# Performance work log

Hardware: AMD Instinct MI355X
Metric: run time of the kernel (lower is better)

Reference implementation:

```python
import jax, jax.numpy as jnp
import numpy as np

CHANNELS = 512
NUM_HEADS = 8
GROUPS = 32
EPS = 1e-5


def setup_inputs() -> dict:
    key = jax.random.key(0)
    ks = jax.random.split(key, 7)
    C = CHANNELS
    x = jax.random.normal(ks[0], (8, C, 32, 32), dtype=jnp.float32)
    gn_weight = jnp.ones((C,), dtype=jnp.float32)
    gn_bias = jnp.zeros((C,), dtype=jnp.float32)
    # Conv1d(C, 3C, k=1) weights ~ N(0, 0.02) per init_weights
    qkv_w = 0.02 * jax.random.normal(ks[1], (3 * C, C), dtype=jnp.float32)
    qkv_b = 0.01 * jax.random.normal(ks[2], (3 * C,), dtype=jnp.float32)
    out_w = 0.02 * jax.random.normal(ks[3], (C, C), dtype=jnp.float32)
    out_b = 0.01 * jax.random.normal(ks[4], (C,), dtype=jnp.float32)
    return {"x": x, "gn_weight": gn_weight, "gn_bias": gn_bias,
            "qkv_w": qkv_w, "qkv_b": qkv_b, "out_w": out_w, "out_b": out_b}


def _forward(x, gn_weight, gn_bias, qkv_w, qkv_b, out_w, out_b):
    n, c, h, w = x.shape
    hw = h * w
    heads = NUM_HEADS
    cph = c // heads
    xs = x.reshape(n, c, hw)  # [N, C, HW]
    # GroupNorm over (channels-in-group, spatial)
    xg = xs.reshape(n, GROUPS, c // GROUPS, hw)
    mean = jnp.mean(xg, axis=(2, 3), keepdims=True)
    var = jnp.var(xg, axis=(2, 3), keepdims=True)
    xn = ((xg - mean) * jax.lax.rsqrt(var + EPS)).reshape(n, c, hw)
    xn = xn * gn_weight[None, :, None] + gn_bias[None, :, None]
    # 1x1 Conv1d QKV projection
    qkv = jnp.einsum('oc,ncl->nol', qkv_w, xn) + qkv_b[None, :, None]  # [N, 3C, HW]
    q, k, v = jnp.split(qkv, 3, axis=1)  # each [N, C, HW]
    q = q.reshape(n * heads, cph, hw)
    k = k.reshape(n * heads, cph, hw)
    v = v.reshape(n * heads, cph, hw)
    scale = 1.0 / np.sqrt(cph).astype(np.float32)
    scores = jnp.einsum('bci,bcj->bij', q, k) * scale  # [NH, HW, HW]
    attn = jax.nn.softmax(scores, axis=-1)
    weighted = jnp.einsum('bij,bcj->bic', attn, v)  # [NH, HW, cph]
    # Faithful to torch: reshape(n, -1, h, w) on [n*heads, hw, cph] layout
    weighted = weighted.reshape(n, c, h, w)
    out = jnp.einsum('oc,nchw->nohw', out_w, weighted) + out_b[None, :, None, None]
    return out


def reference(x, gn_weight, gn_bias, qkv_w, qkv_b, out_w, out_b):
    return _forward(x, gn_weight, gn_bias, qkv_w, qkv_b, out_w, out_b)
```

## Files before the change

### kernel.cpp

```cpp
#include <hip/hip_runtime.h>
#include <math.h>

#define N_    8
#define C_    512
#define HW_   1024
#define G_    32
#define CPG_  16
#define OC3_  1536
#define LOG2E 1.44269504f

typedef _Float16 f16;
typedef f16 f16x8 __attribute__((ext_vector_type(8)));
typedef f16 f16x4 __attribute__((ext_vector_type(4)));
typedef float f32x4 __attribute__((ext_vector_type(4)));

#define GLOAD_LDS16(g, l)                                                          \
    __builtin_amdgcn_global_load_lds(                                              \
        (const __attribute__((address_space(1))) unsigned int*)(const void*)(g),   \
        (__attribute__((address_space(3))) unsigned int*)(void*)(l), 16, 0, 0)

#define WAIT_VM0() __builtin_amdgcn_s_waitcnt(0x0F70)

__global__ __launch_bounds__(256) void prep(const float* __restrict__ x,
                                            const float* __restrict__ gw,
                                            const float* __restrict__ gb,
                                            f16* __restrict__ XT,
                                            const float* __restrict__ qkv_w,
                                            const float* __restrict__ out_w,
                                            const float* __restrict__ qkv_b,
                                            f16* __restrict__ Wq,
                                            f16* __restrict__ Wo,
                                            float* __restrict__ qkv_bs) {
    __shared__ float red1[4], red2[4];
    __shared__ float sm, srstd;
    if (blockIdx.x >= 256) {
        const float QS = 0.125f * LOG2E;
        int idx = (blockIdx.x - 256) * 256 + threadIdx.x;
        if (idx < 786432) {
            float v = qkv_w[idx];
            if (idx < 262144) v *= QS;
            Wq[idx] = (f16)v;
        } else if (idx < 786432 + 262144) {
            Wo[idx - 786432] = (f16)out_w[idx - 786432];
        } else if (idx < 786432 + 262144 + 1536) {
            int i = idx - 786432 - 262144;
            float v = qkv_b[i];
            if (i < 512) v *= QS;
            qkv_bs[i] = v;
        }
        return;
    }
    int blk = blockIdx.x;
    int n = blk >> 5, g = blk & 31;
    size_t base = ((size_t)n * C_ + (size_t)g * CPG_) * HW_;
    const float4* xp4 = (const float4*)(x + base);
    float4 vals[16];
    float s1 = 0.f, s2 = 0.f;
#pragma unroll
    for (int r = 0; r < 16; r++) {
        float4 v = xp4[r * 256 + threadIdx.x];
        vals[r] = v;
        s1 += v.x + v.y + v.z + v.w;
        s2 += v.x * v.x + v.y * v.y + v.z * v.z + v.w * v.w;
    }
#pragma unroll
    for (int off = 32; off > 0; off >>= 1) {
        s1 += __shfl_down(s1, off, 64);
        s2 += __shfl_down(s2, off, 64);
    }
    int wave = threadIdx.x >> 6, lane = threadIdx.x & 63;
    if (lane == 0) { red1[wave] = s1; red2[wave] = s2; }
    __syncthreads();
    if (threadIdx.x == 0) {
        float t1 = red1[0] + red1[1] + red1[2] + red1[3];
        float t2 = red2[0] + red2[1] + red2[2] + red2[3];
        float mean = t1 * (1.f / 16384.f);
        float var  = t2 * (1.f / 16384.f) - mean * mean;
        sm = mean;
        srstd = rsqrtf(var + 1e-5f);
    }
    __syncthreads();
    float mean = sm, rstd = srstd;
    float av[16], bbv[16];
#pragma unroll
    for (int r = 0; r < 16; r++) {
        int c = g * CPG_ + r;
        av[r] = gw[c] * rstd;
        bbv[r] = gb[c] - mean * av[r];
    }
    f16x8 lo[4], hi[4];
#pragma unroll
    for (int r = 0; r < 16; r++) {
        float4 v = vals[r];
        float a = av[r], bb = bbv[r];
        f16 e0 = (f16)(v.x * a + bb), e1 = (f16)(v.y * a + bb);
        f16 e2 = (f16)(v.z * a + bb), e3 = (f16)(v.w * a + bb);
        if (r < 8) { lo[0][r] = e0; lo[1][r] = e1; lo[2][r] = e2; lo[3][r] = e3; }
        else { hi[0][r - 8] = e0; hi[1][r - 8] = e1; hi[2][r - 8] = e2; hi[3][r - 8] = e3; }
    }
    f16* xt = XT + (size_t)n * C_ * HW_ + ((size_t)g * HW_ + threadIdx.x * 4) * 16;
#pragma unroll
    for (int comp = 0; comp < 4; comp++) {
        *(f16x8*)&xt[comp * 16]     = lo[comp];
        *(f16x8*)&xt[comp * 16 + 8] = hi[comp];
    }
}

template <bool FINAL>
__global__ __launch_bounds__(256, 4) void gemm_f16(const f16* __restrict__ A,
                                                   const f16* __restrict__ B,
                                                   const float* __restrict__ bias,
                                                   void* __restrict__ Yq,
                                                   f16* __restrict__ Yv) {
    constexpr int BM = FINAL ? 64 : 128;
    constexpr int MI = BM / 32;
    constexpr int AB = BM * 64;
    __shared__ __align__(16) unsigned char smem[FINAL ? 24576 : 34816];
    int tid = threadIdx.x, lane = tid & 63, w = tid >> 6;
    int m = lane & 15, quad = lane >> 4;
    int ow0 = (w & 1) * (BM / 2), lw0 = (w >> 1) * 64;
    int flat = blockIdx.x;
    int n = flat & 7, rest = flat >> 3;
    int l0 = (rest & 7) * 128, o0 = (rest >> 3) * BM;
    const f16* Bn = B + (size_t)n * C_ * HW_;

    f32x4 acc[MI][4];
#pragma unroll
    for (int i = 0; i < MI; i++)
#pragma unroll
        for (int j = 0; j < 4; j++)
#pragma unroll
            for (int r = 0; r < 4; r++) acc[i][j][r] = 0.f;

#define STAGE_STEP(c0_, pb_)                                                       \
    do {                                                                           \
        _Pragma("unroll")                                                          \
        for (int it = 0; it < BM / 64; it++) {                                     \
            int q = it * 256 + tid;                                                \
            int row = q >> 2, sg = (q & 3) ^ ((row >> 1) & 3);                     \
            GLOAD_LDS16(A + (size_t)(o0 + row) * 512 + (c0_) + sg * 8,             \
                        (f16*)(smem + (pb_) * AB) + (size_t)(it * 256 + w * 64) * 8); \
        }                                                                          \
        _Pragma("unroll")                                                          \
        for (int it = 0; it < 2; it++) {                                           \
            int q = it * 256 + tid;                                                \
            int row = q >> 2, sg = (q & 3) ^ ((row >> 1) & 3);                     \
            size_t baddr;                                                          \
            if (FINAL) {                                                           \
                baddr = (size_t)(l0 + row) * 512 + (c0_) + sg * 8;                 \
            } else {                                                               \
                int c = (c0_) + sg * 8;                                            \
                baddr = ((size_t)(c >> 4) * HW_ + (l0 + row)) * 16 + (c & 15);     \
            }                                                                      \
            GLOAD_LDS16(Bn + baddr,                                                \
                        (f16*)(smem + 2 * AB + (pb_) * 8192) +                     \
                            (size_t)(it * 256 + w * 64) * 8);                      \
        }                                                                          \
    } while (0)

    STAGE_STEP(0, 0);

    for (int cs = 0; cs < 16; cs++) {
        int p = cs & 1;
        WAIT_VM0();
        __syncthreads();
        if (cs < 15) STAGE_STEP((cs + 1) * 32, 1 - p);
        const f16* Asp = (const f16*)(smem + p * AB);
        const f16* Bsp = (const f16*)(smem + 2 * AB + p * 8192);
        f16x8 af[MI], bf[4];
#pragma unroll
        for (int ib = 0; ib < MI; ib++) {
            int row = ow0 + ib * 16 + m;
            int sg = quad ^ ((row >> 1) & 3);
            af[ib] = *(const f16x8*)&Asp[row * 32 + sg * 8];
        }
#pragma unroll
        for (int jb = 0; jb < 4; jb++) {
            int row = lw0 + jb * 16 + m;
            int sg = quad ^ ((row >> 1) & 3);
            bf[jb] = *(const f16x8*)&Bsp[row * 32 + sg * 8];
        }
#pragma unroll
        for (int ib = 0; ib < MI; ib++)
#pragma unroll
            for (int jb = 0; jb < 4; jb++)
                acc[ib][jb] = __builtin_amdgcn_mfma_f32_16x16x32_f16(
                    af[ib], bf[jb], acc[ib][jb], 0, 0, 0);
    }
#undef STAGE_STEP

    float bv[MI][4];
#pragma unroll
    for (int ib = 0; ib < MI; ib++)
#pragma unroll
        for (int r = 0; r < 4; r++)
            bv[ib][r] = bias[o0 + ow0 + ib * 16 + quad * 4 + r];

    if (FINAL) {
        float* on = (float*)Yq + (size_t)n * C_ * HW_;
#pragma unroll
        for (int ib = 0; ib < MI; ib++)
#pragma unroll
            for (int jb = 0; jb < 4; jb++)
#pragma unroll
                for (int r = 0; r < 4; r++)
                    on[(size_t)(o0 + ow0 + ib * 16 + quad * 4 + r) * HW_ +
                       l0 + lw0 + jb * 16 + m] = acc[ib][jb][r] + bv[ib][r];
    } else if (o0 >= 1024) {
        f16* vn = Yv + (size_t)n * C_ * HW_;
#pragma unroll
        for (int ib = 0; ib < MI; ib++)
#pragma unroll
            for (int jb = 0; jb < 4; jb++)
#pragma unroll
                for (int r = 0; r < 4; r++)
                    vn[(size_t)(o0 - 1024 + ow0 + ib * 16 + quad * 4 + r) * HW_ +
                       l0 + lw0 + jb * 16 + m] = (f16)(acc[ib][jb][r] + bv[ib][r]);
    } else {
        __syncthreads();
        f16* T = (f16*)smem;
#pragma unroll
        for (int ib = 0; ib < MI; ib++)
#pragma unroll
            for (int jb = 0; jb < 4; jb++) {
                f16x4 h;
#pragma unroll
                for (int r = 0; r < 4; r++) h[r] = (f16)(acc[ib][jb][r] + bv[ib][r]);
                int l = lw0 + jb * 16 + m;
                int oo = ow0 + ib * 16 + quad * 4;
                *(f16x4*)&T[l * 136 + oo] = h;
            }
        __syncthreads();
        f16* qn = (f16*)Yq + (size_t)n * HW_ * 1024;
#pragma unroll
        for (int rep = 0; rep < 8; rep++) {
            int idx = rep * 256 + tid;
            int l = idx >> 4, seg = idx & 15;
            f16x8 v = *(const f16x8*)&T[l * 136 + seg * 8];
            *(f16x8*)&qn[(size_t)(l0 + l) * 1024 + o0 + seg * 8] = v;
        }
    }
}

__global__ __launch_bounds__(256, 4) void attn_f16(const f16* __restrict__ qkvT,
                                                   const f16* __restrict__ vbuf,
                                                   f16* __restrict__ w2T) {
    __shared__ __align__(16) unsigned char smem[32768];
    f16* Kb0  = (f16*)smem;
    f16* Vb0  = (f16*)(smem + 16384);
    f16* LDSo = (f16*)smem;

    int tid = threadIdx.x;
    int lane = tid & 63, wave = tid >> 6;
    int m = lane & 15, quad = lane >> 4;
    int flat = blockIdx.x;
    int xcd = flat & 7, slot = flat >> 3;
    int itile = slot >> 3, bh = (slot & 7) * 8 + xcd;
    int n = bh >> 3, head = bh & 7;
    int i0 = itile * 64;
    const f16* qb = qkvT + (size_t)n * HW_ * 1024 + head * 64;
    const f16* kb = qb + 512;
    const f16* vb = vbuf + (size_t)n * C_ * HW_ + (size_t)head * 64 * HW_;

    const f16* qr = qb + (size_t)(i0 + wave * 16 + m) * 1024;
    f16x8 aq0 = *(const f16x8*)&qr[quad * 8];
    f16x8 aq1 = *(const f16x8*)&qr[32 + quad * 8];

#pragma unroll
    for (int it = 0; it < 2; it++) {
        int chunk = it * 256 + tid;
        int row = chunk >> 3, seg = chunk & 7;
        int segg = seg ^ (row & 7);
        GLOAD_LDS16(kb + (size_t)row * 1024 + segg * 8,
                    Kb0 + ((size_t)it * 256 + wave * 64) * 8);
        GLOAD_LDS16(vb + (size_t)row * HW_ + segg * 8,
                    Vb0 + ((size_t)it * 256 + wave * 64) * 8);
    }

    f32x4 oacc[4];
#pragma unroll
    for (int cb = 0; cb < 4; cb++)
#pragma unroll
        for (int r = 0; r < 4; r++) oacc[cb][r] = 0.f;
    float lsum = 0.f;
    int m7 = m & 7;

    for (int jt = 0; jt < 16; jt++) {
        int p = jt & 1;
        const f16* Kp = Kb0 + p * 4096;
        const f16* Vp = Vb0 + p * 4096;
        WAIT_VM0();
        __syncthreads();
        if (jt < 15) {
            int j0n = (jt + 1) * 64;
            f16* Kn = Kb0 + (1 - p) * 4096;
            f16* Vn = Vb0 + (1 - p) * 4096;
#pragma unroll
            for (int it = 0; it < 2; it++) {
                int chunk = it * 256 + tid;
                int row = chunk >> 3, seg = chunk & 7;
                int segg = seg ^ (row & 7);
                GLOAD_LDS16(kb + (size_t)(j0n + row) * 1024 + segg * 8,
                            Kn + ((size_t)it * 256 + wave * 64) * 8);
                GLOAD_LDS16(vb + (size_t)row * HW_ + j0n + segg * 8,
                            Vn + ((size_t)it * 256 + wave * 64) * 8);
            }
        }

        f16x8 kf[8];
#pragma unroll
        for (int jb = 0; jb < 4; jb++) {
            int row = jb * 16 + m;
            kf[jb]     = *(const f16x8*)&Kp[row * 64 + ((quad ^ (row & 7)) * 8)];
            kf[4 + jb] = *(const f16x8*)&Kp[row * 64 + (((4 + quad) ^ (row & 7)) * 8)];
        }

        f32x4 sacc[4];
#pragma unroll
        for (int jb = 0; jb < 4; jb++)
#pragma unroll
            for (int r = 0; r < 4; r++) sacc[jb][r] = 0.f;
#pragma unroll
        for (int jb = 0; jb < 4; jb++)
            sacc[jb] = __builtin_amdgcn_mfma_f32_16x16x32_f16(kf[jb], aq0,
                                                              sacc[jb], 0, 0, 0);
#pragma unroll
        for (int jb = 0; jb < 4; jb++)
            sacc[jb] = __builtin_amdgcn_mfma_f32_16x16x32_f16(kf[4 + jb], aq1,
                                                              sacc[jb], 0, 0, 0);

        f16x4 pf[4];
#pragma unroll
        for (int jb = 0; jb < 4; jb++) {
            float p0 = exp2f(sacc[jb][0]), p1 = exp2f(sacc[jb][1]);
            float p2 = exp2f(sacc[jb][2]), p3 = exp2f(sacc[jb][3]);
            lsum += (p0 + p1) + (p2 + p3);
            pf[jb][0] = (f16)p0; pf[jb][1] = (f16)p1;
            pf[jb][2] = (f16)p2; pf[jb][3] = (f16)p3;
        }

#pragma unroll
        for (int jb = 0; jb < 4; jb++) {
            int segb = jb * 2 + (quad >> 1);
#pragma unroll
            for (int cb = 0; cb < 4; cb++) {
                f16x4 vf4 = *(const f16x4*)&Vp[(cb * 16 + m) * 64 +
                                               ((segb ^ m7) * 8) + (quad & 1) * 4];
                oacc[cb] = __builtin_amdgcn_mfma_f32_16x16x16f16(pf[jb], vf4,
                                                                 oacc[cb], 0, 0, 0);
            }
        }
    }

    float ls = lsum;
    ls += __shfl_xor(ls, 16, 64);
    ls += __shfl_xor(ls, 32, 64);
    float linv[4];
#pragma unroll
    for (int r = 0; r < 4; r++) linv[r] = 1.f / __shfl(ls, quad * 4 + r, 64);

    WAIT_VM0();
    __syncthreads();
#pragma unroll
    for (int cb = 0; cb < 4; cb++)
#pragma unroll
        for (int r = 0; r < 4; r++) {
            int sc = (quad * 4 + r) * 64 + cb * 16 + m;
            LDSo[sc * 4 + wave] = (f16)(oacc[cb][r] * linv[r]);
        }
    __syncthreads();
    f16* w2n = w2T + (size_t)n * HW_ * 512;
    int chbase = head * 64 + (i0 >> 4);
#pragma unroll
    for (int it = 0; it < 4; it++) {
        int sc = it * 256 + tid;
        *(f16x4*)&w2n[(size_t)sc * 512 + chbase] = *(const f16x4*)&LDSo[sc * 4];
    }
}

extern "C" void kernel_launch(void* const* d_in, const int* in_sizes, int n_in,
                              void* d_out, int out_size, void* d_ws, size_t ws_size,
                              hipStream_t stream) {
    (void)in_sizes; (void)n_in; (void)out_size; (void)ws_size;
    const float* x     = (const float*)d_in[0];
    const float* gw    = (const float*)d_in[1];
    const float* gb    = (const float*)d_in[2];
    const float* qkv_w = (const float*)d_in[3];
    const float* qkv_b = (const float*)d_in[4];
    const float* out_w = (const float*)d_in[5];
    const float* out_b = (const float*)d_in[6];
    float* out = (float*)d_out;
    char* ws = (char*)d_ws;

    const size_t MB = 1024 * 1024;
    f16*   qkvT   = (f16*)ws;
    f16*   XT     = (f16*)(ws + 16 * MB);
    f16*   vbuf   = (f16*)(ws + 24 * MB);
    f16*   w2T    = (f16*)(ws + 32 * MB);
    f16*   Wq     = (f16*)(ws + 40 * MB);
    f16*   Wo     = (f16*)(ws + 42 * MB);
    float* qkv_bs = (float*)(ws + 43 * MB);

    prep<<<dim3(256 + 4103), 256, 0, stream>>>(x, gw, gb, XT,
                                               qkv_w, out_w, qkv_b, Wq, Wo, qkv_bs);
    gemm_f16<false><<<dim3(768), 256, 0, stream>>>(Wq, XT, qkv_bs, (void*)qkvT, vbuf);
    attn_f16<<<dim3(1024), 256, 0, stream>>>(qkvT, vbuf, w2T);
    gemm_f16<true><<<dim3(512), 256, 0, stream>>>(Wo, w2T, out_b, (void*)out, nullptr);
}
```

Measured before the change: 153.4 us.

## Triple-buffer global-to-LDS loads in GEMM and attention kernels

Both the projection GEMM and the attention kernel move from double to triple-buffered LDS staging. Each loop iteration now waits only until the oldest stage has landed (a partial vmcnt wait) rather than draining all loads, and it prefetches two tiles ahead. The aim is to hide global load latency behind MFMA work. In exchange, LDS per block grows (the attention kernel goes to 48KB), which can lower occupancy, and the raw s_barrier with partial waitcnt needs correct counting of outstanding loads.

```diff
diff --git a/kernel.cpp b/kernel.cpp
--- a/kernel.cpp
+++ b/kernel.cpp
@@ -114,8 +114,10 @@
                                                    f16* __restrict__ Yv) {
     constexpr int BM = FINAL ? 64 : 128;
     constexpr int MI = BM / 32;
-    constexpr int AB = BM * 64;
-    __shared__ __align__(16) unsigned char smem[FINAL ? 24576 : 34816];
+    constexpr int ABUF = BM * 32 * 2;
+    constexpr int BBUF = 128 * 32 * 2;
+    constexpr int G = (BM / 64) + 2;
+    __shared__ __align__(16) unsigned char smem[3 * ABUF + 3 * BBUF];
     int tid = threadIdx.x, lane = tid & 63, w = tid >> 6;
     int m = lane & 15, quad = lane >> 4;
     int ow0 = (w & 1) * (BM / 2), lw0 = (w >> 1) * 64;
@@ -139,7 +141,7 @@
             int q = it * 256 + tid;                                                \
             int row = q >> 2, sg = (q & 3) ^ ((row >> 1) & 3);                     \
             GLOAD_LDS16(A + (size_t)(o0 + row) * 512 + (c0_) + sg * 8,             \
-                        (f16*)(smem + (pb_) * AB) + (size_t)(it * 256 + w * 64) * 8); \
+                        (f16*)(smem + (pb_) * ABUF) + (size_t)(it * 256 + w * 64) * 8); \
         }                                                                          \
         _Pragma("unroll")                                                          \
         for (int it = 0; it < 2; it++) {                                           \
@@ -153,20 +155,22 @@
                 baddr = ((size_t)(c >> 4) * HW_ + (l0 + row)) * 16 + (c & 15);     \
             }                                                                      \
             GLOAD_LDS16(Bn + baddr,                                                \
-                        (f16*)(smem + 2 * AB + (pb_) * 8192) +                     \
+                        (f16*)(smem + 3 * ABUF + (pb_) * BBUF) +                   \
                             (size_t)(it * 256 + w * 64) * 8);                      \
         }                                                                          \
     } while (0)
 
     STAGE_STEP(0, 0);
+    STAGE_STEP(32, 1);
 
     for (int cs = 0; cs < 16; cs++) {
-        int p = cs & 1;
-        WAIT_VM0();
-        __syncthreads();
-        if (cs < 15) STAGE_STEP((cs + 1) * 32, 1 - p);
-        const f16* Asp = (const f16*)(smem + p * AB);
-        const f16* Bsp = (const f16*)(smem + 2 * AB + p * 8192);
+        int p = cs % 3;
+        if (cs < 15) __builtin_amdgcn_s_waitcnt(0x0F70 | G);
+        else         WAIT_VM0();
+        __builtin_amdgcn_s_barrier();
+        if (cs + 2 < 16) STAGE_STEP((cs + 2) * 32, (cs + 2) % 3);
+        const f16* Asp = (const f16*)(smem + p * ABUF);
+        const f16* Bsp = (const f16*)(smem + 3 * ABUF + p * BBUF);
         f16x8 af[MI], bf[4];
 #pragma unroll
         for (int ib = 0; ib < MI; ib++) {
@@ -245,9 +249,7 @@
 __global__ __launch_bounds__(256, 4) void attn_f16(const f16* __restrict__ qkvT,
                                                    const f16* __restrict__ vbuf,
                                                    f16* __restrict__ w2T) {
-    __shared__ __align__(16) unsigned char smem[32768];
-    f16* Kb0  = (f16*)smem;
-    f16* Vb0  = (f16*)(smem + 16384);
+    __shared__ __align__(16) unsigned char smem[49152];
     f16* LDSo = (f16*)smem;
 
     int tid = threadIdx.x;
@@ -266,16 +268,24 @@
     f16x8 aq0 = *(const f16x8*)&qr[quad * 8];
     f16x8 aq1 = *(const f16x8*)&qr[32 + quad * 8];
 
-#pragma unroll
-    for (int it = 0; it < 2; it++) {
-        int chunk = it * 256 + tid;
-        int row = chunk >> 3, seg = chunk & 7;
-        int segg = seg ^ (row & 7);
-        GLOAD_LDS16(kb + (size_t)row * 1024 + segg * 8,
-                    Kb0 + ((size_t)it * 256 + wave * 64) * 8);
-        GLOAD_LDS16(vb + (size_t)row * HW_ + segg * 8,
-                    Vb0 + ((size_t)it * 256 + wave * 64) * 8);
-    }
+#define STAGE_KV(j0_, pb_)                                                         \
+    do {                                                                           \
+        _Pragma("unroll")                                                          \
+        for (int it = 0; it < 2; it++) {                                           \
+            int chunk = it * 256 + tid;                                            \
+            int row = chunk >> 3, seg = chunk & 7;                                 \
+            int segg = seg ^ (row & 7);                                            \
+            GLOAD_LDS16(kb + (size_t)((j0_) + row) * 1024 + segg * 8,              \
+                        (f16*)(smem + (pb_) * 8192) +                              \
+                            ((size_t)it * 256 + wave * 64) * 8);                   \
+            GLOAD_LDS16(vb + (size_t)row * HW_ + (j0_) + segg * 8,                 \
+                        (f16*)(smem + 24576 + (pb_) * 8192) +                      \
+                            ((size_t)it * 256 + wave * 64) * 8);                   \
+        }                                                                          \
+    } while (0)
+
+    STAGE_KV(0, 0);
+    STAGE_KV(64, 1);
 
     f32x4 oacc[4];
 #pragma unroll
@@ -286,26 +296,13 @@
     int m7 = m & 7;
 
     for (int jt = 0; jt < 16; jt++) {
-        int p = jt & 1;
-        const f16* Kp = Kb0 + p * 4096;
-        const f16* Vp = Vb0 + p * 4096;
-        WAIT_VM0();
-        __syncthreads();
-        if (jt < 15) {
-            int j0n = (jt + 1) * 64;
-            f16* Kn = Kb0 + (1 - p) * 4096;
-            f16* Vn = Vb0 + (1 - p) * 4096;
-#pragma unroll
-            for (int it = 0; it < 2; it++) {
-                int chunk = it * 256 + tid;
-                int row = chunk >> 3, seg = chunk & 7;
-                int segg = seg ^ (row & 7);
-                GLOAD_LDS16(kb + (size_t)(j0n + row) * 1024 + segg * 8,
-                            Kn + ((size_t)it * 256 + wave * 64) * 8);
-                GLOAD_LDS16(vb + (size_t)row * HW_ + j0n + segg * 8,
-                            Vn + ((size_t)it * 256 + wave * 64) * 8);
-            }
-        }
+        int p = jt % 3;
+        if (jt < 15) __builtin_amdgcn_s_waitcnt(0x0F74);
+        else         WAIT_VM0();
+        __builtin_amdgcn_s_barrier();
+        if (jt + 2 < 16) STAGE_KV((jt + 2) * 64, (jt + 2) % 3);
+        const f16* Kp = (const f16*)(smem + p * 8192);
+        const f16* Vp = (const f16*)(smem + 24576 + p * 8192);
 
         f16x8 kf[8];
 #pragma unroll
@@ -351,6 +348,7 @@
             }
         }
     }
+#undef STAGE_KV
 
     float ls = lsum;
     ls += __shfl_xor(ls, 16, 64);
```

Measured after the change: 149.0 us. 2.8% less time.
